# Optimization experiments

Measured on AMD Instinct MI355X. Metric: run time of the kernel, lower is better.

The kernel has to match this reference:

```python
import jax, jax.numpy as jnp
import numpy as np
import math

B, S, D, H = 4, 2048, 1024, 16
DK = D // H
DFF = 1024  # FeedForward default d_ff=1024 (DecoderLayer passes only d_model)
EPS = 1e-6
SQRT_2_OVER_PI = math.sqrt(2.0 / math.pi)


def setup_inputs() -> dict:
    key = jax.random.key(0)
    ks = jax.random.split(key, 12)
    sc = 0.02
    x = jax.random.normal(ks[0], (B, S, D), dtype=jnp.float32)
    # causal look-ahead mask: 1 where attendable, 0 where masked
    mask = jnp.broadcast_to(jnp.tril(jnp.ones((S, S), dtype=jnp.int32)), (B, S, S))
    inp = {
        'x': x,
        'mask': mask,
        'Wq': jax.random.normal(ks[1], (D, D), jnp.float32) * sc,
        'bq': jnp.zeros((D,), jnp.float32),
        'Wk': jax.random.normal(ks[2], (D, D), jnp.float32) * sc,
        'bk': jnp.zeros((D,), jnp.float32),
        'Wv': jax.random.normal(ks[3], (D, D), jnp.float32) * sc,
        'bv': jnp.zeros((D,), jnp.float32),
        'Wo': jax.random.normal(ks[4], (D, D), jnp.float32) * sc,
        'bo': jnp.zeros((D,), jnp.float32),
        'W1': jax.random.normal(ks[5], (D, DFF), jnp.float32) * sc,
        'b1': jnp.zeros((DFF,), jnp.float32),
        'W2': jax.random.normal(ks[6], (DFF, D), jnp.float32) * sc,
        'b2': jnp.zeros((D,), jnp.float32),
        'alpha1': jnp.ones((D,), jnp.float32),
        'bias1': jnp.zeros((D,), jnp.float32),
        'alpha2': jnp.ones((D,), jnp.float32),
        'bias2': jnp.zeros((D,), jnp.float32),
    }
    return inp


def _norm(x, alpha, bias):
    # torch: (x - mean) / (x.std(unbiased=True) + eps) * alpha + bias
    mean = jnp.mean(x, axis=-1, keepdims=True)
    var = jnp.sum((x - mean) ** 2, axis=-1, keepdims=True) / (x.shape[-1] - 1)
    std = jnp.sqrt(var)
    return alpha * (x - mean) / (std + EPS) + bias


def _gelu(x):
    return 0.5 * x * (1.0 + jnp.tanh(SQRT_2_OVER_PI * (x + 0.044715 * x ** 3)))


def reference(x, mask, Wq, bq, Wk, bk, Wv, bv, Wo, bo, W1, b1, W2, b2,
              alpha1, bias1, alpha2, bias2):
    b, s, d = x.shape
    x2 = _norm(x, alpha1, bias1)
    q = (x2 @ Wq + bq).reshape(b, s, H, DK).transpose(0, 2, 1, 3)  # bhsd
    k = (x2 @ Wk + bk).reshape(b, s, H, DK).transpose(0, 2, 1, 3)
    v = (x2 @ Wv + bv).reshape(b, s, H, DK).transpose(0, 2, 1, 3)
    scores = jnp.einsum('bhqd,bhkd->bhqk', q, k) / jnp.sqrt(jnp.float32(DK))
    scores = jnp.where(mask[:, None, :, :] == 0, jnp.float32(-1e9), scores)
    probs = jax.nn.softmax(scores, axis=-1)
    attn = jnp.einsum('bhqk,bhkd->bhqd', probs, v)
    concat = attn.transpose(0, 2, 1, 3).reshape(b, s, d)
    x = x + (concat @ Wo + bo)
    x2 = _norm(x, alpha2, bias2)
    ff = _gelu(x2 @ W1 + b1) @ W2 + b2
    return x + ff
```

## Files before the change

### kernel.cpp

```cpp
#include <hip/hip_runtime.h>
#include <hip/hip_bf16.h>
#include <math.h>


#define B_ 4
#define S_ 2048
#define D_ 1024
#define H_ 16
#define DFF_ 1024

typedef __attribute__((ext_vector_type(8))) short short8;
typedef __attribute__((ext_vector_type(8))) unsigned short ushort8;
typedef __attribute__((ext_vector_type(4))) float f32x4;

__device__ __forceinline__ unsigned short f2bf(float f) {
  __hip_bfloat16 h = __float2bfloat16(f);
  return *reinterpret_cast<unsigned short*>(&h);
}

__device__ __forceinline__ void gload16(const void* g, void* l) {
  __builtin_amdgcn_global_load_lds(
      (const __attribute__((address_space(1))) void*)g,
      (__attribute__((address_space(3))) void*)l, 16, 0, 0);
}

__global__ __launch_bounds__(256) void prep_k(
    const float* s0, const float* s1, const float* s2, const float* s3,
    const float* s4, const float* s5, unsigned short* d0, unsigned short* d1,
    unsigned short* d2, unsigned short* d3, unsigned short* d4,
    unsigned short* d5, const float* __restrict__ x,
    const float* __restrict__ alpha, const float* __restrict__ bias,
    unsigned short* __restrict__ xout) {
  __shared__ float tile[64][65];
  const int bid = blockIdx.x;
  const int t = threadIdx.x;
  if (bid < 1536) {
    const int z = bid >> 8, rem = bid & 255;
    const int k0 = (rem >> 4) * 64, n0 = (rem & 15) * 64;
    const float* src;
    unsigned short* dst;
    switch (z) {
      case 0: src = s0; dst = d0; break;
      case 1: src = s1; dst = d1; break;
      case 2: src = s2; dst = d2; break;
      case 3: src = s3; dst = d3; break;
      case 4: src = s4; dst = d4; break;
      default: src = s5; dst = d5; break;
    }
    const int r = t >> 2, c0 = (t & 3) * 16;
    const float4* sp = reinterpret_cast<const float4*>(
        src + (size_t)(k0 + r) * 1024 + n0 + c0);
#pragma unroll
    for (int j = 0; j < 4; ++j) {
      float4 v = sp[j];
      tile[r][c0 + 4 * j] = v.x;
      tile[r][c0 + 4 * j + 1] = v.y;
      tile[r][c0 + 4 * j + 2] = v.z;
      tile[r][c0 + 4 * j + 3] = v.w;
    }
    __syncthreads();
    ushort8 o0, o1;
#pragma unroll
    for (int j = 0; j < 8; ++j) o0[j] = f2bf(tile[c0 + j][r]);
#pragma unroll
    for (int j = 0; j < 8; ++j) o1[j] = f2bf(tile[c0 + 8 + j][r]);
    unsigned short* dp = dst + (size_t)(n0 + r) * 1024 + k0 + c0;
    *reinterpret_cast<ushort8*>(dp) = o0;
    *reinterpret_cast<ushort8*>(dp + 8) = o1;
  } else {
    const int w = t >> 6, lane = t & 63;
    const int row = (bid - 1536) * 4 + w;
    const float4* xp = reinterpret_cast<const float4*>(x + (size_t)row * D_);
    const float4* ap = reinterpret_cast<const float4*>(alpha);
    const float4* bp = reinterpret_cast<const float4*>(bias);
    float4 v[4];
    float s = 0.0f, q = 0.0f;
#pragma unroll
    for (int j = 0; j < 4; ++j) {
      v[j] = xp[lane + 64 * j];
      s += v[j].x + v[j].y + v[j].z + v[j].w;
      q += v[j].x * v[j].x + v[j].y * v[j].y + v[j].z * v[j].z +
           v[j].w * v[j].w;
    }
#pragma unroll
    for (int off = 1; off < 64; off <<= 1) {
      s += __shfl_xor(s, off);
      q += __shfl_xor(q, off);
    }
    const float mean = s * (1.0f / D_);
    const float var = fmaxf((q - D_ * mean * mean) * (1.0f / (D_ - 1)), 0.0f);
    const float inv = 1.0f / (sqrtf(var) + 1e-6f);
    ushort4* op = reinterpret_cast<ushort4*>(xout + (size_t)row * D_);
#pragma unroll
    for (int j = 0; j < 4; ++j) {
      float4 a = ap[lane + 64 * j];
      float4 b = bp[lane + 64 * j];
      ushort4 o;
      o.x = f2bf((v[j].x - mean) * inv * a.x + b.x);
      o.y = f2bf((v[j].y - mean) * inv * a.y + b.y);
      o.z = f2bf((v[j].z - mean) * inv * a.z + b.z);
      o.w = f2bf((v[j].w - mean) * inv * a.w + b.w);
      op[lane + 64 * j] = o;
    }
  }
}

__global__ __launch_bounds__(256) void ln_k(const float* __restrict__ x,
                                            const float* __restrict__ alpha,
                                            const float* __restrict__ bias,
                                            unsigned short* __restrict__ out) {
  const int w = threadIdx.x >> 6, lane = threadIdx.x & 63;
  const int row = blockIdx.x * 4 + w;
  const float4* xp = reinterpret_cast<const float4*>(x + (size_t)row * D_);
  const float4* ap = reinterpret_cast<const float4*>(alpha);
  const float4* bp = reinterpret_cast<const float4*>(bias);
  float4 v[4];
  float s = 0.0f, q = 0.0f;
#pragma unroll
  for (int j = 0; j < 4; ++j) {
    v[j] = xp[lane + 64 * j];
    s += v[j].x + v[j].y + v[j].z + v[j].w;
    q += v[j].x * v[j].x + v[j].y * v[j].y + v[j].z * v[j].z + v[j].w * v[j].w;
  }
#pragma unroll
  for (int off = 1; off < 64; off <<= 1) {
    s += __shfl_xor(s, off);
    q += __shfl_xor(q, off);
  }
  const float mean = s * (1.0f / D_);
  const float var = fmaxf((q - D_ * mean * mean) * (1.0f / (D_ - 1)), 0.0f);
  const float inv = 1.0f / (sqrtf(var) + 1e-6f);
  ushort4* op = reinterpret_cast<ushort4*>(out + (size_t)row * D_);
#pragma unroll
  for (int j = 0; j < 4; ++j) {
    float4 a = ap[lane + 64 * j];
    float4 b = bp[lane + 64 * j];
    ushort4 o;
    o.x = f2bf((v[j].x - mean) * inv * a.x + b.x);
    o.y = f2bf((v[j].y - mean) * inv * a.y + b.y);
    o.z = f2bf((v[j].z - mean) * inv * a.z + b.z);
    o.w = f2bf((v[j].w - mean) * inv * a.w + b.w);
    op[lane + 64 * j] = o;
  }
}

__device__ __forceinline__ void gemm_core64(
    const unsigned short* __restrict__ A, const unsigned short* __restrict__ Wt,
    int m0, int n0, int K, unsigned short* As ,
    unsigned short* Bs , f32x4 (&acc)[2][4]) {
  const int t = threadIdx.x;
  const int wv = t >> 6, lane = t & 63, quad = lane >> 4, l16 = lane & 15;
  const int wm = wv >> 1, wn = wv & 1;
  const int lr8 = lane >> 3;
  const int lseg = ((lane & 7) ^ lr8) * 8;

  const unsigned short* Ag0 = A + (size_t)(m0 + wv * 16 + lr8) * K + lseg;
  const unsigned short* Ag1 = A + (size_t)(m0 + wv * 16 + 8 + lr8) * K + lseg;
  const unsigned short* Bg0 = Wt + (size_t)(n0 + wv * 32 + lr8) * K + lseg;
  const unsigned short* Bg1 = Wt + (size_t)(n0 + wv * 32 + 8 + lr8) * K + lseg;
  const unsigned short* Bg2 = Wt + (size_t)(n0 + wv * 32 + 16 + lr8) * K + lseg;
  const unsigned short* Bg3 = Wt + (size_t)(n0 + wv * 32 + 24 + lr8) * K + lseg;
  unsigned short* Al0 = &As[(wv * 16) * 64];
  unsigned short* Al1 = &As[(wv * 16 + 8) * 64];
  unsigned short* Bl0 = &Bs[(wv * 32) * 64];
  unsigned short* Bl1 = &Bs[(wv * 32 + 8) * 64];
  unsigned short* Bl2 = &Bs[(wv * 32 + 16) * 64];
  unsigned short* Bl3 = &Bs[(wv * 32 + 24) * 64];

  for (int k0 = 0; k0 < K; k0 += 64) {
    gload16(Ag0, Al0);
    gload16(Ag1, Al1);
    gload16(Bg0, Bl0);
    gload16(Bg1, Bl1);
    gload16(Bg2, Bl2);
    gload16(Bg3, Bl3);
    __syncthreads();
    short8 af[2][2], bf[2][4];
#pragma unroll
    for (int p = 0; p < 2; ++p) {
#pragma unroll
      for (int mt = 0; mt < 2; ++mt) {
        int r = wm * 32 + mt * 16 + l16;
        af[p][mt] = *reinterpret_cast<const short8*>(
            &As[r * 64 + (((p * 4 + quad) ^ (r & 7)) << 3)]);
      }
#pragma unroll
      for (int nt = 0; nt < 4; ++nt) {
        int r = wn * 64 + nt * 16 + l16;
        bf[p][nt] = *reinterpret_cast<const short8*>(
            &Bs[r * 64 + (((p * 4 + quad) ^ (r & 7)) << 3)]);
      }
    }
#pragma unroll
    for (int p = 0; p < 2; ++p)
#pragma unroll
      for (int mt = 0; mt < 2; ++mt)
#pragma unroll
        for (int nt = 0; nt < 4; ++nt)
          acc[mt][nt] = __builtin_amdgcn_mfma_f32_16x16x32_bf16(
              af[p][mt], bf[p][nt], acc[mt][nt], 0, 0, 0);
    __syncthreads();
    Ag0 += 64; Ag1 += 64; Bg0 += 64; Bg1 += 64; Bg2 += 64; Bg3 += 64;
  }
}

__global__ __launch_bounds__(256, 6) void gemm_k(
    const unsigned short* __restrict__ A, const unsigned short* __restrict__ Wt,
    const float* __restrict__ bias, const float* __restrict__ res,
    void* __restrict__ outp, int M, int N, int K, int flags) {
  __shared__ unsigned short As[64 * 64];
  __shared__ unsigned short Bs[128 * 64];
  const int t = threadIdx.x;
  const int m0 = blockIdx.y * 64, n0 = blockIdx.x * 128;
  const int wv = t >> 6, lane = t & 63, quad = lane >> 4, l16 = lane & 15;
  const int wm = wv >> 1, wn = wv & 1;
  f32x4 acc[2][4] = {};
  gemm_core64(A, Wt, m0, n0, K, As, Bs, acc);

  const bool obf = flags & 1, dog = flags & 2;
#pragma unroll
  for (int nt = 0; nt < 4; ++nt) {
    int col = n0 + wn * 64 + nt * 16 + l16;
    float bv = bias[col];
#pragma unroll
    for (int mt = 0; mt < 2; ++mt) {
#pragma unroll
      for (int r = 0; r < 4; ++r) {
        int row = m0 + wm * 32 + mt * 16 + quad * 4 + r;
        float v = acc[mt][nt][r] + bv;
        if (res) v += res[(size_t)row * N + col];
        if (dog) {
          float e = __expf(1.5957691216057308f * (v + 0.044715f * v * v * v));
          float th = 1.0f - 2.0f / (1.0f + e);
          v = 0.5f * v * (1.0f + th);
        }
        if (obf)
          ((unsigned short*)outp)[(size_t)row * N + col] = f2bf(v);
        else
          ((float*)outp)[(size_t)row * N + col] = v;
      }
    }
  }
}

__global__ __launch_bounds__(256, 4) void gemmqkv_k(
    const unsigned short* __restrict__ A, const unsigned short* __restrict__ Wt,
    const float* __restrict__ bq, const float* __restrict__ bk,
    const float* __restrict__ bv, unsigned short* __restrict__ outq,
    unsigned short* __restrict__ outk, unsigned short* __restrict__ outvt,
    int M, int K) {
  __shared__ unsigned short As[64 * 64];
  __shared__ unsigned short Bs[128 * 64];
  const int t = threadIdx.x;
  const int m0 = blockIdx.y * 64, n0 = blockIdx.x * 128;
  const int wv = t >> 6, lane = t & 63, quad = lane >> 4, l16 = lane & 15;
  const int wm = wv >> 1, wn = wv & 1;
  f32x4 acc[2][4] = {};
  gemm_core64(A, Wt, m0, n0, K, As, Bs, acc);

  const int seg = n0 >> 10;
  const int nb = n0 & 1023;
  const float* bias = (seg == 0) ? bq : (seg == 1) ? bk : bv;
  if (seg < 2) {
    unsigned short* o = (seg == 0) ? outq : outk;
#pragma unroll
    for (int nt = 0; nt < 4; ++nt) {
      int col = nb + wn * 64 + nt * 16 + l16;
      float bvv = bias[col];
#pragma unroll
      for (int mt = 0; mt < 2; ++mt)
#pragma unroll
        for (int r = 0; r < 4; ++r) {
          int row = m0 + wm * 32 + mt * 16 + quad * 4 + r;
          o[(size_t)row * D_ + col] = f2bf(acc[mt][nt][r] + bvv);
        }
    }
  } else {
#pragma unroll
    for (int nt = 0; nt < 4; ++nt) {
      int col = nb + wn * 64 + nt * 16 + l16;
      float bvv = bias[col];
      int h = col >> 6, dk = col & 63;
#pragma unroll
      for (int mt = 0; mt < 2; ++mt) {
        int m = m0 + wm * 32 + mt * 16 + quad * 4;
        int b = m >> 11, sidx = m & 2047;
        ushort4 o;
        o.x = f2bf(acc[mt][nt][0] + bvv);
        o.y = f2bf(acc[mt][nt][1] + bvv);
        o.z = f2bf(acc[mt][nt][2] + bvv);
        o.w = f2bf(acc[mt][nt][3] + bvv);
        *reinterpret_cast<ushort4*>(
            &outvt[(((size_t)(b * 16 + h) * 64 + dk) * 2048 + sidx)]) = o;
      }
    }
  }
}

__global__ __launch_bounds__(256, 3) void attn_k(
    const unsigned short* __restrict__ Q, const unsigned short* __restrict__ Kg,
    const unsigned short* __restrict__ VT, unsigned short* __restrict__ Og) {
  __shared__ unsigned short Ks[2][64 * 64];
  __shared__ unsigned short Vs[2][64 * 64];
  __shared__ unsigned short Ps[4 * 16 * 72];
  const int t = threadIdx.x;
  const int qt = 31 - (blockIdx.x >> 6);
  const int bh = blockIdx.x & 63;
  const int b = bh >> 4, h = bh & 15;
  const int w = t >> 6, lane = t & 63, quad = lane >> 4, l16 = lane & 15;
  const int q0 = qt * 64 + w * 16;
  unsigned short* PsW = &Ps[w * 16 * 72];

  short8 qf[2];
#pragma unroll
  for (int kc = 0; kc < 2; ++kc)
    qf[kc] = *reinterpret_cast<const short8*>(
        Q + (size_t)(b * S_ + q0 + l16) * D_ + h * 64 + kc * 32 + quad * 8);
  asm volatile("" ::"v"(qf[0]), "v"(qf[1]) : "memory");

  f32x4 Oh[4] = {};
  f32x4 sums = {};
  short8 onev;
#pragma unroll
  for (int j = 0; j < 8; ++j) onev[j] = (short)0x3F80;

  const int srA = w * 8 + (lane >> 3);
  const int ssA = ((lane & 7) ^ (srA & 7)) * 8;
  const int srB = srA + 32;
  const int ssB = ((lane & 7) ^ (srB & 7)) * 8;
  const unsigned short* KgA = Kg + (size_t)(b * S_ + srA) * D_ + h * 64 + ssA;
  const unsigned short* KgB = Kg + (size_t)(b * S_ + srB) * D_ + h * 64 + ssB;
  const unsigned short* VgA = VT + ((size_t)bh * 64 + srA) * 2048 + ssA;
  const unsigned short* VgB = VT + ((size_t)bh * 64 + srB) * 2048 + ssB;
  unsigned short* KlA = &Ks[0][(w * 8) * 64];
  unsigned short* KlB = &Ks[0][(32 + w * 8) * 64];
  unsigned short* VlA = &Vs[0][(w * 8) * 64];
  unsigned short* VlB = &Vs[0][(32 + w * 8) * 64];

  const float C0 = 0.18033688011f;
  const float C1 = -23.08312065f;

  gload16(KgA, KlA);
  gload16(KgB, KlB);
  gload16(VgA, VlA);
  gload16(VgB, VlB);
  KgA += (size_t)64 * D_;
  KgB += (size_t)64 * D_;
  VgA += 64;
  VgB += 64;

  for (int kt = 0; kt <= qt; ++kt) {
    const bool diag = (kt == qt);
    const int coff = (kt & 1) << 12;
    const int noff = ((kt & 1) ^ 1) << 12;

    if (kt < qt) {
      gload16(KgA, KlA + noff);
      gload16(KgB, KlB + noff);
      gload16(VgA, VlA + noff);
      gload16(VgB, VlB + noff);
      KgA += (size_t)64 * D_;
      KgB += (size_t)64 * D_;
      VgA += 64;
      VgB += 64;
      asm volatile("s_waitcnt vmcnt(4)" ::: "memory");
    } else {
      asm volatile("s_waitcnt vmcnt(0)" ::: "memory");
    }
    asm volatile("s_barrier" ::: "memory");

    const unsigned short* Ksc = &Ks[0][coff];
    const unsigned short* Vsc = &Vs[0][coff];

    f32x4 sch[4] = {};
    __builtin_amdgcn_s_setprio(1);
#pragma unroll
    for (int mt = 0; mt < 4; ++mt) {
      int r = mt * 16 + l16;
      short8 kf0 = *reinterpret_cast<const short8*>(
          &Ksc[r * 64 + ((quad ^ (r & 7)) << 3)]);
      short8 kf1 = *reinterpret_cast<const short8*>(
          &Ksc[r * 64 + (((4 + quad) ^ (r & 7)) << 3)]);
      sch[mt] = __builtin_amdgcn_mfma_f32_16x16x32_bf16(kf0, qf[0], sch[mt],
                                                        0, 0, 0);
      sch[mt] = __builtin_amdgcn_mfma_f32_16x16x32_bf16(kf1, qf[1], sch[mt],
                                                        0, 0, 0);
    }
    __builtin_amdgcn_s_setprio(0);

    {
      const int kb0 = kt * 64;
      const int q = q0 + l16;
#pragma unroll
      for (int mt = 0; mt < 4; ++mt) {
        float pv[4];
#pragma unroll
        for (int r = 0; r < 4; ++r) {
          int key = kb0 + mt * 16 + quad * 4 + r;
          float p = __builtin_amdgcn_exp2f(fmaf(sch[mt][r], C0, C1));
          if (diag && key > q) p = 0.0f;
          pv[r] = p;
        }
        ushort4 pk = {f2bf(pv[0]), f2bf(pv[1]), f2bf(pv[2]), f2bf(pv[3])};
        *reinterpret_cast<ushort4*>(&PsW[l16 * 72 + mt * 16 + quad * 4]) = pk;
      }
    }
    __builtin_amdgcn_sched_barrier(0);

    short8 pf[2];
#pragma unroll
    for (int kc = 0; kc < 2; ++kc)
      pf[kc] = *reinterpret_cast<const short8*>(
          &PsW[l16 * 72 + kc * 32 + quad * 8]);

    __builtin_amdgcn_s_setprio(1);
#pragma unroll
    for (int kc = 0; kc < 2; ++kc) {
      sums = __builtin_amdgcn_mfma_f32_16x16x32_bf16(pf[kc], onev, sums,
                                                     0, 0, 0);
#pragma unroll
      for (int nd = 0; nd < 4; ++nd) {
        int r = nd * 16 + l16;
        short8 vf = *reinterpret_cast<const short8*>(
            &Vsc[r * 64 + (((kc * 4 + quad) ^ (r & 7)) << 3)]);
        Oh[nd] = __builtin_amdgcn_mfma_f32_16x16x32_bf16(pf[kc], vf, Oh[nd],
                                                         0, 0, 0);
      }
    }
    __builtin_amdgcn_s_setprio(0);
    asm volatile("s_barrier" ::: "memory");
  }

#pragma unroll
  for (int r = 0; r < 4; ++r) {
    float rl = 1.0f / sums[r];
#pragma unroll
    for (int nd = 0; nd < 4; ++nd)
      Og[(size_t)(b * S_ + q0 + quad * 4 + r) * D_ + h * 64 + nd * 16 + l16] =
          f2bf(Oh[nd][r] * rl);
  }
}

extern "C" void kernel_launch(void* const* d_in, const int* in_sizes, int n_in,
                              void* d_out, int out_size, void* d_ws,
                              size_t ws_size, hipStream_t stream) {
  const float* x = (const float*)d_in[0];
  const float* Wq = (const float*)d_in[2];
  const float* bq = (const float*)d_in[3];
  const float* Wk = (const float*)d_in[4];
  const float* bk = (const float*)d_in[5];
  const float* Wv = (const float*)d_in[6];
  const float* bv = (const float*)d_in[7];
  const float* Wo = (const float*)d_in[8];
  const float* bo = (const float*)d_in[9];
  const float* W1 = (const float*)d_in[10];
  const float* b1 = (const float*)d_in[11];
  const float* W2 = (const float*)d_in[12];
  const float* b2 = (const float*)d_in[13];
  const float* alpha1 = (const float*)d_in[14];
  const float* bias1 = (const float*)d_in[15];
  const float* alpha2 = (const float*)d_in[16];
  const float* bias2 = (const float*)d_in[17];
  float* out = (float*)d_out;

  char* ws = (char*)d_ws;
  const size_t MB = 1024 * 1024;
  unsigned short* wqT = (unsigned short*)(ws + 0 * MB);
  unsigned short* wkT = (unsigned short*)(ws + 2 * MB);
  unsigned short* wvT = (unsigned short*)(ws + 4 * MB);
  unsigned short* woT = (unsigned short*)(ws + 6 * MB);
  unsigned short* w1T = (unsigned short*)(ws + 8 * MB);
  unsigned short* w2T = (unsigned short*)(ws + 10 * MB);
  unsigned short* x2a = (unsigned short*)(ws + 12 * MB);
  unsigned short* qb = (unsigned short*)(ws + 28 * MB);
  unsigned short* kb = (unsigned short*)(ws + 44 * MB);
  unsigned short* vtb = (unsigned short*)(ws + 60 * MB);

  const int M = B_ * S_;

  prep_k<<<dim3(1536 + M / 4), dim3(256), 0, stream>>>(
      Wq, Wk, Wv, Wo, W1, W2, wqT, wkT, wvT, woT, w1T, w2T, x, alpha1, bias1,
      x2a);

  gemmqkv_k<<<dim3(24, 128), dim3(256), 0, stream>>>(x2a, wqT, bq, bk, bv, qb,
                                                     kb, vtb, M, D_);

  attn_k<<<dim3(2048), dim3(256), 0, stream>>>(qb, kb, vtb, x2a);

  dim3 gg(D_ / 128, M / 64);
  gemm_k<<<gg, dim3(256), 0, stream>>>(x2a, woT, bo, x, out, M, D_, D_, 0);

  ln_k<<<dim3(M / 4), dim3(256), 0, stream>>>(out, alpha2, bias2, qb);

  gemm_k<<<gg, dim3(256), 0, stream>>>(qb, w1T, b1, nullptr, kb, M, DFF_, D_, 3);

  gemm_k<<<gg, dim3(256), 0, stream>>>(kb, w2T, b2, out, out, M, D_, DFF_, 0);
}
```

Measured before the change: 399.4 us.

## Triple-buffer GEMM with 256x128 tiles and XCD-aware block mapping

Replaces the single-buffered 64x128 GEMM core with a 256x128 tile computed by 512 threads. It uses a three-stage LDS ring in dynamic shared memory, with async global-to-LDS loads issued two k-steps ahead and explicit vmcnt waits. Loads are interleaved between MFMA half-steps, and MFMA sections run at raised wave priority. Block indices are remapped so each XCD works on contiguous M tiles, improving L2 reuse. The cost is 144KB of LDS per block, which limits occupancy to one block per CU, and fewer, larger grids that may leave CUs with uneven load.

```diff
diff --git a/kernel.cpp b/kernel.cpp
--- a/kernel.cpp
+++ b/kernel.cpp
@@ -8,6 +8,7 @@
 #define D_ 1024
 #define H_ 16
 #define DFF_ 1024
+#define BUFS 24576
 
 typedef __attribute__((ext_vector_type(8))) short short8;
 typedef __attribute__((ext_vector_type(8))) unsigned short ushort8;
@@ -144,78 +145,139 @@
   }
 }
 
-__device__ __forceinline__ void gemm_core64(
+__device__ __forceinline__ void gemm_core8p(
     const unsigned short* __restrict__ A, const unsigned short* __restrict__ Wt,
-    int m0, int n0, int K, unsigned short* As ,
-    unsigned short* Bs , f32x4 (&acc)[2][4]) {
+    int m0, int n0, int K, unsigned short* lds, f32x4 (&acc)[4][4]) {
   const int t = threadIdx.x;
   const int wv = t >> 6, lane = t & 63, quad = lane >> 4, l16 = lane & 15;
   const int wm = wv >> 1, wn = wv & 1;
-  const int lr8 = lane >> 3;
-  const int lseg = ((lane & 7) ^ lr8) * 8;
-
-  const unsigned short* Ag0 = A + (size_t)(m0 + wv * 16 + lr8) * K + lseg;
-  const unsigned short* Ag1 = A + (size_t)(m0 + wv * 16 + 8 + lr8) * K + lseg;
-  const unsigned short* Bg0 = Wt + (size_t)(n0 + wv * 32 + lr8) * K + lseg;
-  const unsigned short* Bg1 = Wt + (size_t)(n0 + wv * 32 + 8 + lr8) * K + lseg;
-  const unsigned short* Bg2 = Wt + (size_t)(n0 + wv * 32 + 16 + lr8) * K + lseg;
-  const unsigned short* Bg3 = Wt + (size_t)(n0 + wv * 32 + 24 + lr8) * K + lseg;
-  unsigned short* Al0 = &As[(wv * 16) * 64];
-  unsigned short* Al1 = &As[(wv * 16 + 8) * 64];
-  unsigned short* Bl0 = &Bs[(wv * 32) * 64];
-  unsigned short* Bl1 = &Bs[(wv * 32 + 8) * 64];
-  unsigned short* Bl2 = &Bs[(wv * 32 + 16) * 64];
-  unsigned short* Bl3 = &Bs[(wv * 32 + 24) * 64];
-
-  for (int k0 = 0; k0 < K; k0 += 64) {
-    gload16(Ag0, Al0);
-    gload16(Ag1, Al1);
-    gload16(Bg0, Bl0);
-    gload16(Bg1, Bl1);
-    gload16(Bg2, Bl2);
-    gload16(Bg3, Bl3);
-    __syncthreads();
-    short8 af[2][2], bf[2][4];
-#pragma unroll
-    for (int p = 0; p < 2; ++p) {
-#pragma unroll
-      for (int mt = 0; mt < 2; ++mt) {
-        int r = wm * 32 + mt * 16 + l16;
-        af[p][mt] = *reinterpret_cast<const short8*>(
-            &As[r * 64 + (((p * 4 + quad) ^ (r & 7)) << 3)]);
+  const int NT = K >> 6;
+
+  const unsigned short* Ag[4];
+  int Ao[4];
+  const unsigned short* Bg[2];
+  int Bo[2];
+#pragma unroll
+  for (int g = 0; g < 4; ++g) {
+    int u = g * 512 + t, row = u >> 3, ps = u & 7;
+    Ag[g] = A + (size_t)(m0 + row) * K + ((ps ^ (row & 7)) << 3);
+    Ao[g] = u * 8;
+  }
+#pragma unroll
+  for (int g = 0; g < 2; ++g) {
+    int u = g * 512 + t, row = u >> 3, ps = u & 7;
+    Bg[g] = Wt + (size_t)(n0 + row) * K + ((ps ^ (row & 7)) << 3);
+    Bo[g] = 16384 + u * 8;
+  }
+
+#pragma unroll
+  for (int tt = 0; tt < 2; ++tt) {
+    unsigned short* lb = lds + tt * BUFS;
+    const int kk = tt * 64;
+    gload16(Ag[0] + kk, lb + Ao[0]);
+    gload16(Ag[1] + kk, lb + Ao[1]);
+    gload16(Bg[0] + kk, lb + Bo[0]);
+    gload16(Ag[2] + kk, lb + Ao[2]);
+    gload16(Ag[3] + kk, lb + Ao[3]);
+    gload16(Bg[1] + kk, lb + Bo[1]);
+  }
+
+  int cb = 0;
+  for (int kt = 0; kt < NT; ++kt) {
+    if (kt + 1 < NT)
+      asm volatile("s_waitcnt vmcnt(6)" ::: "memory");
+    else
+      asm volatile("s_waitcnt vmcnt(0)" ::: "memory");
+    asm volatile("s_barrier" ::: "memory");
+
+    const unsigned short* Ab = lds + cb * BUFS;
+    const unsigned short* Bb = Ab + 16384;
+    int sbf = cb + 2;
+    if (sbf >= 3) sbf -= 3;
+    unsigned short* sb = lds + sbf * BUFS;
+    const int kk2 = (kt + 2) << 6;
+    const bool st = (kt + 2 < NT);
+
+    {
+      short8 af[4], bf[4];
+#pragma unroll
+      for (int mt = 0; mt < 4; ++mt) {
+        int r = wm * 64 + mt * 16 + l16;
+        af[mt] = *reinterpret_cast<const short8*>(
+            &Ab[r * 64 + ((quad ^ (r & 7)) << 3)]);
       }
 #pragma unroll
       for (int nt = 0; nt < 4; ++nt) {
         int r = wn * 64 + nt * 16 + l16;
-        bf[p][nt] = *reinterpret_cast<const short8*>(
-            &Bs[r * 64 + (((p * 4 + quad) ^ (r & 7)) << 3)]);
-      }
-    }
-#pragma unroll
-    for (int p = 0; p < 2; ++p)
-#pragma unroll
-      for (int mt = 0; mt < 2; ++mt)
+        bf[nt] = *reinterpret_cast<const short8*>(
+            &Bb[r * 64 + ((quad ^ (r & 7)) << 3)]);
+      }
+      if (st) {
+        gload16(Ag[0] + kk2, sb + Ao[0]);
+        gload16(Ag[1] + kk2, sb + Ao[1]);
+        gload16(Bg[0] + kk2, sb + Bo[0]);
+      }
+      __builtin_amdgcn_sched_barrier(0);
+      __builtin_amdgcn_s_setprio(1);
+#pragma unroll
+      for (int mt = 0; mt < 4; ++mt)
 #pragma unroll
         for (int nt = 0; nt < 4; ++nt)
           acc[mt][nt] = __builtin_amdgcn_mfma_f32_16x16x32_bf16(
-              af[p][mt], bf[p][nt], acc[mt][nt], 0, 0, 0);
-    __syncthreads();
-    Ag0 += 64; Ag1 += 64; Bg0 += 64; Bg1 += 64; Bg2 += 64; Bg3 += 64;
-  }
-}
-
-__global__ __launch_bounds__(256, 6) void gemm_k(
+              af[mt], bf[nt], acc[mt][nt], 0, 0, 0);
+      __builtin_amdgcn_s_setprio(0);
+      __builtin_amdgcn_sched_barrier(0);
+    }
+    {
+      short8 af[4], bf[4];
+#pragma unroll
+      for (int mt = 0; mt < 4; ++mt) {
+        int r = wm * 64 + mt * 16 + l16;
+        af[mt] = *reinterpret_cast<const short8*>(
+            &Ab[r * 64 + (((4 + quad) ^ (r & 7)) << 3)]);
+      }
+#pragma unroll
+      for (int nt = 0; nt < 4; ++nt) {
+        int r = wn * 64 + nt * 16 + l16;
+        bf[nt] = *reinterpret_cast<const short8*>(
+            &Bb[r * 64 + (((4 + quad) ^ (r & 7)) << 3)]);
+      }
+      if (st) {
+        gload16(Ag[2] + kk2, sb + Ao[2]);
+        gload16(Ag[3] + kk2, sb + Ao[3]);
+        gload16(Bg[1] + kk2, sb + Bo[1]);
+      }
+      __builtin_amdgcn_sched_barrier(0);
+      __builtin_amdgcn_s_setprio(1);
+#pragma unroll
+      for (int mt = 0; mt < 4; ++mt)
+#pragma unroll
+        for (int nt = 0; nt < 4; ++nt)
+          acc[mt][nt] = __builtin_amdgcn_mfma_f32_16x16x32_bf16(
+              af[mt], bf[nt], acc[mt][nt], 0, 0, 0);
+      __builtin_amdgcn_s_setprio(0);
+      __builtin_amdgcn_sched_barrier(0);
+    }
+    asm volatile("s_barrier" ::: "memory");
+    cb = (cb + 1 == 3) ? 0 : cb + 1;
+  }
+}
+
+__global__ __launch_bounds__(512, 2) void gemm_k(
     const unsigned short* __restrict__ A, const unsigned short* __restrict__ Wt,
     const float* __restrict__ bias, const float* __restrict__ res,
     void* __restrict__ outp, int M, int N, int K, int flags) {
-  __shared__ unsigned short As[64 * 64];
-  __shared__ unsigned short Bs[128 * 64];
+  extern __shared__ unsigned short lds[];
   const int t = threadIdx.x;
-  const int m0 = blockIdx.y * 64, n0 = blockIdx.x * 128;
+  const int bid = blockIdx.x;
+  const int xcd = bid & 7, loc = bid >> 3;
+  const int n_blk = loc >> 2;
+  const int m_blk = xcd * 4 + (loc & 3);
+  const int m0 = m_blk * 256, n0 = n_blk * 128;
   const int wv = t >> 6, lane = t & 63, quad = lane >> 4, l16 = lane & 15;
   const int wm = wv >> 1, wn = wv & 1;
-  f32x4 acc[2][4] = {};
-  gemm_core64(A, Wt, m0, n0, K, As, Bs, acc);
+  f32x4 acc[4][4] = {};
+  gemm_core8p(A, Wt, m0, n0, K, lds, acc);
 
   const bool obf = flags & 1, dog = flags & 2;
 #pragma unroll
@@ -223,10 +285,10 @@
     int col = n0 + wn * 64 + nt * 16 + l16;
     float bv = bias[col];
 #pragma unroll
-    for (int mt = 0; mt < 2; ++mt) {
+    for (int mt = 0; mt < 4; ++mt) {
 #pragma unroll
       for (int r = 0; r < 4; ++r) {
-        int row = m0 + wm * 32 + mt * 16 + quad * 4 + r;
+        int row = m0 + wm * 64 + mt * 16 + quad * 4 + r;
         float v = acc[mt][nt][r] + bv;
         if (res) v += res[(size_t)row * N + col];
         if (dog) {
@@ -243,20 +305,23 @@
   }
 }
 
-__global__ __launch_bounds__(256, 4) void gemmqkv_k(
+__global__ __launch_bounds__(512, 2) void gemmqkv_k(
     const unsigned short* __restrict__ A, const unsigned short* __restrict__ Wt,
     const float* __restrict__ bq, const float* __restrict__ bk,
     const float* __restrict__ bv, unsigned short* __restrict__ outq,
     unsigned short* __restrict__ outk, unsigned short* __restrict__ outvt,
     int M, int K) {
-  __shared__ unsigned short As[64 * 64];
-  __shared__ unsigned short Bs[128 * 64];
+  extern __shared__ unsigned short lds[];
   const int t = threadIdx.x;
-  const int m0 = blockIdx.y * 64, n0 = blockIdx.x * 128;
+  const int bid = blockIdx.x;
+  const int xcd = bid & 7, loc = bid >> 3;
+  const int n_blk = loc >> 2;
+  const int m_blk = xcd * 4 + (loc & 3);
+  const int m0 = m_blk * 256, n0 = n_blk * 128;
   const int wv = t >> 6, lane = t & 63, quad = lane >> 4, l16 = lane & 15;
   const int wm = wv >> 1, wn = wv & 1;
-  f32x4 acc[2][4] = {};
-  gemm_core64(A, Wt, m0, n0, K, As, Bs, acc);
+  f32x4 acc[4][4] = {};
+  gemm_core8p(A, Wt, m0, n0, K, lds, acc);
 
   const int seg = n0 >> 10;
   const int nb = n0 & 1023;
@@ -268,10 +333,10 @@
       int col = nb + wn * 64 + nt * 16 + l16;
       float bvv = bias[col];
 #pragma unroll
-      for (int mt = 0; mt < 2; ++mt)
+      for (int mt = 0; mt < 4; ++mt)
 #pragma unroll
         for (int r = 0; r < 4; ++r) {
-          int row = m0 + wm * 32 + mt * 16 + quad * 4 + r;
+          int row = m0 + wm * 64 + mt * 16 + quad * 4 + r;
           o[(size_t)row * D_ + col] = f2bf(acc[mt][nt][r] + bvv);
         }
     }
@@ -282,8 +347,8 @@
       float bvv = bias[col];
       int h = col >> 6, dk = col & 63;
 #pragma unroll
-      for (int mt = 0; mt < 2; ++mt) {
-        int m = m0 + wm * 32 + mt * 16 + quad * 4;
+      for (int mt = 0; mt < 4; ++mt) {
+        int m = m0 + wm * 64 + mt * 16 + quad * 4;
         int b = m >> 11, sidx = m & 2047;
         ushort4 o;
         o.x = f2bf(acc[mt][nt][0] + bvv);
@@ -476,23 +541,36 @@
   unsigned short* kb = (unsigned short*)(ws + 44 * MB);
   unsigned short* vtb = (unsigned short*)(ws + 60 * MB);
 
+  static bool attr_set = false;
+  if (!attr_set) {
+    attr_set = true;
+    (void)hipFuncSetAttribute((const void*)gemm_k,
+                              hipFuncAttributeMaxDynamicSharedMemorySize,
+                              147456);
+    (void)hipFuncSetAttribute((const void*)gemmqkv_k,
+                              hipFuncAttributeMaxDynamicSharedMemorySize,
+                              147456);
+  }
+
   const int M = B_ * S_;
 
   prep_k<<<dim3(1536 + M / 4), dim3(256), 0, stream>>>(
       Wq, Wk, Wv, Wo, W1, W2, wqT, wkT, wvT, woT, w1T, w2T, x, alpha1, bias1,
       x2a);
 
-  gemmqkv_k<<<dim3(24, 128), dim3(256), 0, stream>>>(x2a, wqT, bq, bk, bv, qb,
-                                                     kb, vtb, M, D_);
+  gemmqkv_k<<<dim3(768), dim3(512), 147456, stream>>>(x2a, wqT, bq, bk, bv,
+                                                      qb, kb, vtb, M, D_);
 
   attn_k<<<dim3(2048), dim3(256), 0, stream>>>(qb, kb, vtb, x2a);
 
-  dim3 gg(D_ / 128, M / 64);
-  gemm_k<<<gg, dim3(256), 0, stream>>>(x2a, woT, bo, x, out, M, D_, D_, 0);
+  gemm_k<<<dim3(256), dim3(512), 147456, stream>>>(x2a, woT, bo, x, out, M,
+                                                   D_, D_, 0);
 
   ln_k<<<dim3(M / 4), dim3(256), 0, stream>>>(out, alpha2, bias2, qb);
 
-  gemm_k<<<gg, dim3(256), 0, stream>>>(qb, w1T, b1, nullptr, kb, M, DFF_, D_, 3);
-
-  gemm_k<<<gg, dim3(256), 0, stream>>>(kb, w2T, b2, out, out, M, D_, DFF_, 0);
-}
+  gemm_k<<<dim3(256), dim3(512), 147456, stream>>>(qb, w1T, b1, nullptr, kb,
+                                                   M, DFF_, D_, 3);
+
+  gemm_k<<<dim3(256), dim3(512), 147456, stream>>>(kb, w2T, b2, out, out, M,
+                                                   D_, DFF_, 0);
+}
```

Result: no change. 392.2 us (-1.8%).
